# Optimization experiments

Measured on AMD Instinct MI355X. Metric: run time of the kernel, lower is better.

Reference implementation:

```python
import jax, jax.numpy as jnp
import numpy as np

N, E, B = 20000, 160000, 64
NFEAT, NHID, HEADS, NCLASS = 128, 64, 16, 10
GAT_SLOPE = 0.2    # LeakyReLU inside GATv2 attention
OUT_SLOPE = 0.01   # torch.nn.functional.leaky_relu default
TEMPERATURE = 1.0


def _lrelu(x, slope):
    return jnp.where(x >= 0, x, slope * x)


def gatv2_conv(x, src, dst, Wl, bl, Wr, br, att, bias):
    # x: [N, Fin]; PyG GATv2Conv with share_weights=False, concat=False (mean over heads)
    xl = (x @ Wl + bl).reshape(N, HEADS, NHID)   # source-side transform
    xr = (x @ Wr + br).reshape(N, HEADS, NHID)   # target-side transform
    e = _lrelu(xl[src] + xr[dst], GAT_SLOPE)     # [E', H, C] per-edge pre-activation
    logit = jnp.einsum('ehc,hc->eh', e, att)     # [E', H]
    # segment softmax over incoming edges of each target node (self-loops guarantee >=1 edge)
    m = jax.ops.segment_max(logit, dst, num_segments=N)
    m = jnp.where(jnp.isfinite(m), m, 0.0)
    ex = jnp.exp(logit - m[dst])
    den = jax.ops.segment_sum(ex, dst, num_segments=N)
    alpha = ex / den[dst]                        # [E', H]
    out = jax.ops.segment_sum(alpha[:, :, None] * xl[src], dst, num_segments=N)  # [N, H, C]
    return out.mean(axis=1) + bias               # concat=False -> head average, then bias


def setup_inputs() -> dict:
    key = jax.random.key(0)
    ks = jax.random.split(key, 20)
    s = 0.05
    inp = {
        'x': jax.random.normal(ks[0], (N, NFEAT), dtype=jnp.float32),
        'edge_index': jax.random.randint(ks[1], (2, E), 0, N, dtype=jnp.int64)
            if jax.config.jax_enable_x64 else jax.random.randint(ks[1], (2, E), 0, N).astype(jnp.int32),
        'batch': jnp.sort(jax.random.randint(ks[2], (N,), 0, B)).astype(jnp.int32),
        # GATv2 layer 1
        'W1l': jax.random.normal(ks[3], (NFEAT, HEADS * NHID), dtype=jnp.float32) * s,
        'b1l': jnp.zeros((HEADS * NHID,), jnp.float32),
        'W1r': jax.random.normal(ks[4], (NFEAT, HEADS * NHID), dtype=jnp.float32) * s,
        'b1r': jnp.zeros((HEADS * NHID,), jnp.float32),
        'att1': jax.random.normal(ks[5], (HEADS, NHID), dtype=jnp.float32) * s,
        'bias1': jnp.zeros((NHID,), jnp.float32),
        # GATv2 layer 2
        'W2l': jax.random.normal(ks[6], (NHID, HEADS * NHID), dtype=jnp.float32) * s,
        'b2l': jnp.zeros((HEADS * NHID,), jnp.float32),
        'W2r': jax.random.normal(ks[7], (NHID, HEADS * NHID), dtype=jnp.float32) * s,
        'b2r': jnp.zeros((HEADS * NHID,), jnp.float32),
        'att2': jax.random.normal(ks[8], (HEADS, NHID), dtype=jnp.float32) * s,
        'bias2': jnp.zeros((NHID,), jnp.float32),
        # heads
        'Wc': jax.random.normal(ks[9], (NHID, NCLASS), dtype=jnp.float32) * s,
        'bc': jnp.zeros((NCLASS,), jnp.float32),
        'Wv': jax.random.normal(ks[10], (NHID, 1), dtype=jnp.float32) * s,
        'bv': jnp.zeros((1,), jnp.float32),
    }
    return inp


def reference(x, edge_index, batch, W1l, b1l, W1r, b1r, att1, bias1,
              W2l, b2l, W2r, b2r, att2, bias2, Wc, bc, Wv, bv):
    loop = jnp.arange(N, dtype=edge_index.dtype)  # PyG add_self_loops=True
    src = jnp.concatenate([edge_index[0], loop])
    dst = jnp.concatenate([edge_index[1], loop])

    h = _lrelu(gatv2_conv(x, src, dst, W1l, b1l, W1r, b1r, att1, bias1), OUT_SLOPE)
    h = _lrelu(gatv2_conv(h, src, dst, W2l, b2l, W2r, b2r, att2, bias2), OUT_SLOPE)
    # dropout p=0.0 -> identity

    sums = jax.ops.segment_sum(h, batch, num_segments=B)           # [B, NHID]
    cnt = jax.ops.segment_sum(jnp.ones((N,), h.dtype), batch, num_segments=B)
    pooled = sums / jnp.maximum(cnt, 1.0)[:, None]                 # global_mean_pool

    logits = (pooled @ Wc + bc) / TEMPERATURE                      # [B, NCLASS]
    log_var = pooled @ Wv + bv                                     # [B, 1]
    return (logits, log_var)
```

## Files before the change

kernel.cpp:

```cpp
#include <hip/hip_runtime.h>
#include <hip/hip_bf16.h>
#include <hip/hip_fp16.h>
#include <math.h>

#define NN   20000
#define EE   160000
#define NBAT 64
#define NF   128
#define NH   64
#define NHEAD 16
#define NCLS 10
#define ETOT (EE + NN)

typedef __attribute__((ext_vector_type(8))) short short8;
typedef __attribute__((ext_vector_type(8))) _Float16 half8;
typedef __attribute__((ext_vector_type(2))) _Float16 h2;
typedef __attribute__((ext_vector_type(4))) float f32x4;
typedef unsigned short ushort_t;

#if __has_builtin(__builtin_amdgcn_fdot2)
typedef __fp16 fdot2_t __attribute__((ext_vector_type(2)));
static __device__ __forceinline__ float dot2(h2 a, h2 b, float c) {
    return __builtin_amdgcn_fdot2(__builtin_bit_cast(fdot2_t, a),
                                  __builtin_bit_cast(fdot2_t, b), c, false);
}
#else
static __device__ __forceinline__ float dot2(h2 a, h2 b, float c) {
    return c + (float)a.x * (float)b.x + (float)a.y * (float)b.y;
}
#endif

static __device__ __forceinline__ ushort_t f2bf_rn(float x) {
    unsigned u = __builtin_bit_cast(unsigned, x);
    unsigned r = (u + 0x7fffu + ((u >> 16) & 1u)) >> 16;
    return (ushort_t)r;
}
static __device__ __forceinline__ float bf2f(ushort_t u) {
    unsigned v = (unsigned)u << 16;
    return __builtin_bit_cast(float, v);
}

__global__ void k_hist(const int* __restrict__ ei, int* __restrict__ deg) {
    int e = blockIdx.x * 256 + threadIdx.x;
    if (e < EE) atomicAdd(&deg[ei[EE + e]], 1);
}

__global__ void k_scan(const int* __restrict__ deg, int* __restrict__ rowptr,
                       int* __restrict__ cursor, int* __restrict__ csr) {
    const int T = 1024, PER = (NN + T - 1) / T;
    __shared__ int part[T];
    int t = threadIdx.x;
    int local[PER];
    int s = 0;
    #pragma unroll
    for (int i = 0; i < PER; ++i) {
        int idx = t * PER + i;
        int v = (idx < NN) ? deg[idx] : 0;
        local[i] = v; s += v;
    }
    part[t] = s;
    __syncthreads();
    for (int off = 1; off < T; off <<= 1) {
        int v = (t >= off) ? part[t - off] : 0;
        __syncthreads();
        part[t] += v;
        __syncthreads();
    }
    int ex = (t == 0) ? 0 : part[t - 1];
    #pragma unroll
    for (int i = 0; i < PER; ++i) {
        int idx = t * PER + i;
        if (idx < NN) {
            int base = ex + idx;
            rowptr[idx] = base;
            csr[base]   = idx;
            cursor[idx] = base + 1;
            ex += local[i];
        }
    }
    if (t == T - 1) rowptr[NN] = ex + NN;
}

__global__ void k_scatter(const int* __restrict__ ei, int* __restrict__ cursor,
                          int* __restrict__ csr) {
    int e = blockIdx.x * 256 + threadIdx.x;
    if (e >= EE) return;
    int s = ei[e], d = ei[EE + e];
    int pos = atomicAdd(&cursor[d], 1);
    csr[pos] = s;
}

__global__ void k_bounds(const int* __restrict__ batch, int* __restrict__ bstart) {
    int n = blockIdx.x * 256 + threadIdx.x;
    if (n >= NN) return;
    int b = batch[n];
    if (n == 0) for (int bb = 0; bb <= b; ++bb) bstart[bb] = 0;
    int bn = (n + 1 < NN) ? batch[n + 1] : NBAT;
    for (int bb = b + 1; bb <= bn; ++bb) bstart[bb] = n + 1;
}

__global__ void k_split_a(const float* __restrict__ A, ushort_t* __restrict__ hi,
                          ushort_t* __restrict__ lo, int count4) {
    int idx = blockIdx.x * 256 + threadIdx.x;
    if (idx >= count4) return;
    float4 x = *(const float4*)(A + idx * 4);
    ushort4 h, l;
    h.x = f2bf_rn(x.x); l.x = f2bf_rn(x.x - bf2f(h.x));
    h.y = f2bf_rn(x.y); l.y = f2bf_rn(x.y - bf2f(h.y));
    h.z = f2bf_rn(x.z); l.z = f2bf_rn(x.z - bf2f(h.z));
    h.w = f2bf_rn(x.w); l.w = f2bf_rn(x.w - bf2f(h.w));
    *(ushort4*)(hi + idx * 4) = h;
    *(ushort4*)(lo + idx * 4) = l;
}

template<int K>
__global__ void k_split_w(const float* __restrict__ W, ushort_t* __restrict__ hi,
                          ushort_t* __restrict__ lo) {
    int idx = blockIdx.x * 256 + threadIdx.x;
    if (idx >= K * 1024) return;
    int k = idx >> 10, n = idx & 1023;
    float x = W[idx];
    ushort_t h = f2bf_rn(x);
    hi[n * K + k] = h;
    lo[n * K + k] = f2bf_rn(x - bf2f(h));
}

template<int K>
__global__ __launch_bounds__(256) void k_gemm_mfma(
    const ushort_t* __restrict__ Ahi, const ushort_t* __restrict__ Alo, int M,
    const ushort_t* __restrict__ W0hi, const ushort_t* __restrict__ W0lo,
    const float* __restrict__ b0, _Float16* __restrict__ O0,
    const ushort_t* __restrict__ W1hi, const ushort_t* __restrict__ W1lo,
    const float* __restrict__ b1, _Float16* __restrict__ O1)
{
    const ushort_t* Whi = blockIdx.z ? W1hi : W0hi;
    const ushort_t* Wlo = blockIdx.z ? W1lo : W0lo;
    const float*    bi  = blockIdx.z ? b1 : b0;
    _Float16*       O   = blockIdx.z ? O1 : O0;

    const int c0 = blockIdx.x * 128;
    const int r0 = blockIdx.y * 128;

    __shared__ __align__(16) ushort_t As_hi[128 * 64];
    __shared__ __align__(16) ushort_t As_lo[128 * 64];
    __shared__ __align__(16) ushort_t Ws_hi[128 * 64];
    __shared__ __align__(16) ushort_t Ws_lo[128 * 64];

    const int t = threadIdx.x;
    const int lane = t & 63;
    const int wv = t >> 6, wr = wv >> 1, wc = wv & 1;
    const int fr = lane & 15;
    const int k0 = (lane >> 4) * 8;

    f32x4 acc[4][4] = {};

    for (int kt = 0; kt < K; kt += 64) {
        #pragma unroll
        for (int p = 0; p < 4; ++p) {
            int idx = p * 256 + t;
            int m  = idx >> 3;
            int kc = (idx & 7) * 8;
            int gr = r0 + m;
            uint4 vh = make_uint4(0, 0, 0, 0), vl = make_uint4(0, 0, 0, 0);
            if (gr < M) {
                vh = *(const uint4*)(Ahi + (size_t)gr * K + kt + kc);
                vl = *(const uint4*)(Alo + (size_t)gr * K + kt + kc);
            }
            int sw = (m * 128 + kc * 2) ^ ((m & 7) << 4);
            *(uint4*)((char*)As_hi + sw) = vh;
            *(uint4*)((char*)As_lo + sw) = vl;
            uint4 wh = *(const uint4*)(Whi + (size_t)(c0 + m) * K + kt + kc);
            uint4 wl = *(const uint4*)(Wlo + (size_t)(c0 + m) * K + kt + kc);
            *(uint4*)((char*)Ws_hi + sw) = wh;
            *(uint4*)((char*)Ws_lo + sw) = wl;
        }
        __syncthreads();

        #pragma unroll
        for (int ks = 0; ks < 64; ks += 32) {
            short8 ah[4], al[4], bh[4], bl[4];
            #pragma unroll
            for (int i = 0; i < 4; ++i) {
                int row = wr * 64 + i * 16 + fr;
                int off = (row * 128 + (ks + k0) * 2) ^ ((row & 7) << 4);
                ah[i] = *(const short8*)((const char*)As_hi + off);
                al[i] = *(const short8*)((const char*)As_lo + off);
            }
            #pragma unroll
            for (int j = 0; j < 4; ++j) {
                int col = wc * 64 + j * 16 + fr;
                int off = (col * 128 + (ks + k0) * 2) ^ ((col & 7) << 4);
                bh[j] = *(const short8*)((const char*)Ws_hi + off);
                bl[j] = *(const short8*)((const char*)Ws_lo + off);
            }
            #pragma unroll
            for (int i = 0; i < 4; ++i)
                #pragma unroll
                for (int j = 0; j < 4; ++j) {
                    acc[i][j] = __builtin_amdgcn_mfma_f32_16x16x32_bf16(ah[i], bh[j], acc[i][j], 0, 0, 0);
                    acc[i][j] = __builtin_amdgcn_mfma_f32_16x16x32_bf16(ah[i], bl[j], acc[i][j], 0, 0, 0);
                    acc[i][j] = __builtin_amdgcn_mfma_f32_16x16x32_bf16(al[i], bh[j], acc[i][j], 0, 0, 0);
                }
        }
        __syncthreads();
    }

    float bj[4];
    #pragma unroll
    for (int j = 0; j < 4; ++j) bj[j] = bi[c0 + wc * 64 + j * 16 + fr];
    #pragma unroll
    for (int i = 0; i < 4; ++i) {
        int rbase = r0 + wr * 64 + i * 16 + (lane >> 4) * 4;
        #pragma unroll
        for (int r = 0; r < 4; ++r) {
            int gr = rbase + r;
            if (gr < M) {
                #pragma unroll
                for (int j = 0; j < 4; ++j)
                    O[(size_t)gr * 1024 + c0 + wc * 64 + j * 16 + fr] =
                        (_Float16)(acc[i][j][r] + bj[j]);
            }
        }
    }
}

static __device__ __forceinline__ void edge_update(
    half8 a0, half8 a1, half8 xr0, half8 xr1, const h2* att2,
    float& m, float& den, float* acc)
{
    half8 t0 = a0 + xr0;
    half8 t1 = a1 + xr1;
    t0 = __builtin_elementwise_max(t0, t0 * (_Float16)0.2f);
    t1 = __builtin_elementwise_max(t1, t1 * (_Float16)0.2f);
    const h2* p0 = (const h2*)&t0;
    const h2* p1 = (const h2*)&t1;
    float lg = 0.f;
    #pragma unroll
    for (int j = 0; j < 4; ++j) lg = dot2(p0[j], att2[j], lg);
    #pragma unroll
    for (int j = 0; j < 4; ++j) lg = dot2(p1[j], att2[4 + j], lg);
    lg += __shfl_xor(lg, 1);
    lg += __shfl_xor(lg, 2);
    const float nm = fmaxf(m, lg);
    const float p  = __expf(lg - nm);
    const float sc = __expf(m - nm);
    den = den * sc + p;
    const _Float16* xa = (const _Float16*)&a0;
    const _Float16* xb = (const _Float16*)&a1;
    #pragma unroll
    for (int j = 0; j < 8; ++j) acc[j]     = fmaf((float)xa[j], p, acc[j] * sc);
    #pragma unroll
    for (int j = 0; j < 8; ++j) acc[8 + j] = fmaf((float)xb[j], p, acc[8 + j] * sc);
    m = nm;
}

template<int SPLIT>
__global__ __launch_bounds__(256) void k_attn(
    const _Float16* __restrict__ xl, const _Float16* __restrict__ xr,
    const float* __restrict__ att, const float* __restrict__ bias,
    const int* __restrict__ rowptr, const int* __restrict__ csr,
    float* __restrict__ hout, ushort_t* __restrict__ hhi, ushort_t* __restrict__ hlo)
{
    const int wave = threadIdx.x >> 6;
    const int lane = threadIdx.x & 63;
    const int n = blockIdx.x * 4 + wave;
    if (n >= NN) return;
    const int h  = lane >> 2;
    const int cc = lane & 3;
    const int cb = h * NH + cc * 16;

    h2 att2[8];
    #pragma unroll
    for (int i = 0; i < 4; ++i) {
        float4 a = *(const float4*)(att + cb + i * 4);
        att2[i * 2 + 0] = h2{(_Float16)a.x, (_Float16)a.y};
        att2[i * 2 + 1] = h2{(_Float16)a.z, (_Float16)a.w};
    }
    const half8 xr0 = *(const half8*)(xr + (size_t)n * 1024 + cb);
    const half8 xr1 = *(const half8*)(xr + (size_t)n * 1024 + cb + 8);

    float acc[16];
    #pragma unroll
    for (int j = 0; j < 16; ++j) acc[j] = 0.f;
    float m = -INFINITY, den = 0.f;

    const int e0 = rowptr[n], e1 = rowptr[n + 1];
    int e = e0;
    for (; e + 4 <= e1; e += 4) {
        const int s0 = csr[e], s1 = csr[e + 1], s2 = csr[e + 2], s3 = csr[e + 3];
        const _Float16* p0 = xl + (size_t)s0 * 1024 + cb;
        const _Float16* p1 = xl + (size_t)s1 * 1024 + cb;
        const _Float16* p2 = xl + (size_t)s2 * 1024 + cb;
        const _Float16* p3 = xl + (size_t)s3 * 1024 + cb;
        half8 a0 = *(const half8*)p0, a1 = *(const half8*)(p0 + 8);
        half8 b0 = *(const half8*)p1, b1 = *(const half8*)(p1 + 8);
        half8 c0 = *(const half8*)p2, c1 = *(const half8*)(p2 + 8);
        half8 d0 = *(const half8*)p3, d1 = *(const half8*)(p3 + 8);
        edge_update(a0, a1, xr0, xr1, att2, m, den, acc);
        edge_update(b0, b1, xr0, xr1, att2, m, den, acc);
        edge_update(c0, c1, xr0, xr1, att2, m, den, acc);
        edge_update(d0, d1, xr0, xr1, att2, m, den, acc);
    }
    for (; e < e1; ++e) {
        const int s = csr[e];
        const _Float16* p0 = xl + (size_t)s * 1024 + cb;
        half8 a0 = *(const half8*)p0, a1 = *(const half8*)(p0 + 8);
        edge_update(a0, a1, xr0, xr1, att2, m, den, acc);
    }

    const float inv = 1.f / den;
    float v[16];
    #pragma unroll
    for (int j = 0; j < 16; ++j) v[j] = acc[j] * inv;
    #pragma unroll
    for (int mask = 4; mask <= 32; mask <<= 1)
        #pragma unroll
        for (int j = 0; j < 16; ++j) v[j] += __shfl_xor(v[j], mask);

    if (h == 0) {
        float bvv[16];
        #pragma unroll
        for (int i = 0; i < 4; ++i)
            *(float4*)(bvv + i * 4) = *(const float4*)(bias + cc * 16 + i * 4);
        #pragma unroll
        for (int i = 0; i < 4; ++i) {
            float o[4];
            #pragma unroll
            for (int r = 0; r < 4; ++r) {
                float tt = v[i * 4 + r] * 0.0625f + bvv[i * 4 + r];
                o[r] = fmaxf(tt, 0.01f * tt);
            }
            if (SPLIT) {
                ushort4 hh, ll;
                hh.x = f2bf_rn(o[0]); ll.x = f2bf_rn(o[0] - bf2f(hh.x));
                hh.y = f2bf_rn(o[1]); ll.y = f2bf_rn(o[1] - bf2f(hh.y));
                hh.z = f2bf_rn(o[2]); ll.z = f2bf_rn(o[2] - bf2f(hh.z));
                hh.w = f2bf_rn(o[3]); ll.w = f2bf_rn(o[3] - bf2f(hh.w));
                *(ushort4*)(hhi + (size_t)n * NH + cc * 16 + i * 4) = hh;
                *(ushort4*)(hlo + (size_t)n * NH + cc * 16 + i * 4) = ll;
            } else {
                *(float4*)(hout + (size_t)n * NH + cc * 16 + i * 4) =
                    make_float4(o[0], o[1], o[2], o[3]);
            }
        }
    }
}

#define PNODES 128
__global__ __launch_bounds__(256) void k_pool_partial(
    const float* __restrict__ h2buf, const int* __restrict__ batch,
    float* __restrict__ sums)
{
    const int n0 = blockIdx.x * PNODES;
    const int c = threadIdx.x & 63;
    const int r = threadIdx.x >> 6;
    const int nend = (n0 + PNODES < NN) ? n0 + PNODES : NN;
    float s = 0.f;
    int bcur = -1;
    for (int n = n0 + r; n < nend; n += 4) {
        int b = batch[n];
        if (b != bcur) {
            if (bcur >= 0) atomicAdd(&sums[bcur * NH + c], s);
            bcur = b; s = 0.f;
        }
        s += h2buf[(size_t)n * NH + c];
    }
    if (bcur >= 0) atomicAdd(&sums[bcur * NH + c], s);
}

__global__ void k_heads(const float* __restrict__ sums, const int* __restrict__ bstart,
                        const float* __restrict__ Wc, const float* __restrict__ bc,
                        const float* __restrict__ Wv, const float* __restrict__ bv,
                        float* __restrict__ out)
{
    const int b = blockIdx.x, c = threadIdx.x;
    const float cnt = (float)(bstart[b + 1] - bstart[b]);
    const float pooled = sums[b * NH + c] / fmaxf(cnt, 1.f);
    __shared__ float pl[NH];
    pl[c] = pooled;
    __syncthreads();
    if (c < NCLS) {
        float a = bc[c];
        for (int k = 0; k < NH; ++k) a = fmaf(pl[k], Wc[k * NCLS + c], a);
        out[b * NCLS + c] = a;
    } else if (c == NCLS) {
        float a = bv[0];
        for (int k = 0; k < NH; ++k) a = fmaf(pl[k], Wv[k], a);
        out[NBAT * NCLS + b] = a;
    }
}

extern "C" void kernel_launch(void* const* d_in, const int* in_sizes, int n_in,
                              void* d_out, int out_size, void* d_ws, size_t ws_size,
                              hipStream_t stream)
{
    const float* x     = (const float*)d_in[0];
    const int*   ei    = (const int*)  d_in[1];
    const int*   batch = (const int*)  d_in[2];
    const float* W1l = (const float*)d_in[3],  *b1l = (const float*)d_in[4];
    const float* W1r = (const float*)d_in[5],  *b1r = (const float*)d_in[6];
    const float* att1 = (const float*)d_in[7], *bias1 = (const float*)d_in[8];
    const float* W2l = (const float*)d_in[9],  *b2l = (const float*)d_in[10];
    const float* W2r = (const float*)d_in[11], *b2r = (const float*)d_in[12];
    const float* att2 = (const float*)d_in[13], *bias2 = (const float*)d_in[14];
    const float* Wc = (const float*)d_in[15],  *bc = (const float*)d_in[16];
    const float* Wv = (const float*)d_in[17],  *bv = (const float*)d_in[18];
    float* out = (float*)d_out;

    char* ws = (char*)d_ws;
    size_t off = 0;
    auto carve = [&](size_t bytes) {
        char* p = ws + off;
        off = (off + bytes + 255) & ~(size_t)255;
        return p;
    };
    _Float16* xl    = (_Float16*)carve((size_t)NN * 1024 * 2);
    _Float16* xr    = (_Float16*)carve((size_t)NN * 1024 * 2);
    float*    h2b   = (float*)carve((size_t)NN * NH * 4);
    float*    psums = (float*)carve((size_t)NBAT * NH * 4);
    ushort_t* Axhi  = (ushort_t*)carve((size_t)NN * NF * 2);
    ushort_t* Axlo  = (ushort_t*)carve((size_t)NN * NF * 2);
    ushort_t* h1hi  = (ushort_t*)carve((size_t)NN * NH * 2);
    ushort_t* h1lo  = (ushort_t*)carve((size_t)NN * NH * 2);
    ushort_t* Wt1lh = (ushort_t*)carve((size_t)1024 * NF * 2);
    ushort_t* Wt1ll = (ushort_t*)carve((size_t)1024 * NF * 2);
    ushort_t* Wt1rh = (ushort_t*)carve((size_t)1024 * NF * 2);
    ushort_t* Wt1rl = (ushort_t*)carve((size_t)1024 * NF * 2);
    ushort_t* Wt2lh = (ushort_t*)carve((size_t)1024 * NH * 2);
    ushort_t* Wt2ll = (ushort_t*)carve((size_t)1024 * NH * 2);
    ushort_t* Wt2rh = (ushort_t*)carve((size_t)1024 * NH * 2);
    ushort_t* Wt2rl = (ushort_t*)carve((size_t)1024 * NH * 2);
    int*      deg    = (int*)carve((size_t)NN * 4);
    int*      cursor = (int*)carve((size_t)NN * 4);
    int*      rowptr = (int*)carve((size_t)(NN + 1) * 4);
    int*      csr    = (int*)carve((size_t)ETOT * 4);
    int*      bstart = (int*)carve((size_t)(NBAT + 1) * 4);

    hipMemsetAsync(deg, 0, (size_t)NN * 4, stream);
    k_hist   <<<(EE + 255) / 256, 256, 0, stream>>>(ei, deg);
    k_scan   <<<1, 1024, 0, stream>>>(deg, rowptr, cursor, csr);
    k_scatter<<<(EE + 255) / 256, 256, 0, stream>>>(ei, cursor, csr);
    k_bounds <<<(NN + 255) / 256, 256, 0, stream>>>(batch, bstart);

    k_split_a<<<(NN * NF / 4 + 255) / 256, 256, 0, stream>>>(x, Axhi, Axlo, NN * NF / 4);
    k_split_w<NF><<<(NF * 1024 + 255) / 256, 256, 0, stream>>>(W1l, Wt1lh, Wt1ll);
    k_split_w<NF><<<(NF * 1024 + 255) / 256, 256, 0, stream>>>(W1r, Wt1rh, Wt1rl);
    k_split_w<NH><<<(NH * 1024 + 255) / 256, 256, 0, stream>>>(W2l, Wt2lh, Wt2ll);
    k_split_w<NH><<<(NH * 1024 + 255) / 256, 256, 0, stream>>>(W2r, Wt2rh, Wt2rl);

    const int MB = (NN + 127) / 128;
    k_gemm_mfma<NF><<<dim3(8, MB, 2), 256, 0, stream>>>(
        Axhi, Axlo, NN, Wt1lh, Wt1ll, b1l, xl, Wt1rh, Wt1rl, b1r, xr);
    k_attn<1><<<NN / 4, 256, 0, stream>>>(xl, xr, att1, bias1, rowptr, csr,
                                          (float*)nullptr, h1hi, h1lo);
    k_gemm_mfma<NH><<<dim3(8, MB, 2), 256, 0, stream>>>(
        h1hi, h1lo, NN, Wt2lh, Wt2ll, b2l, xl, Wt2rh, Wt2rl, b2r, xr);
    k_attn<0><<<NN / 4, 256, 0, stream>>>(xl, xr, att2, bias2, rowptr, csr,
                                          h2b, (ushort_t*)nullptr, (ushort_t*)nullptr);
    hipMemsetAsync(psums, 0, (size_t)NBAT * NH * 4, stream);
    k_pool_partial<<<(NN + PNODES - 1) / PNODES, 256, 0, stream>>>(h2b, batch, psums);
    k_heads<<<NBAT, NH, 0, stream>>>(psums, bstart, Wc, bc, Wv, bv, out);
}
```

Baseline: 394.4 us.

## Fuse input bf16 split into GEMM, batch weight splits, drop online softmax max

Layer-1 GEMM now reads fp32 x directly and splits it into bf16 hi/lo in the tile loader, removing the separate split kernel and its intermediate buffers. The four weight-split launches are merged into one launch. GEMM grid order is swapped so blocks iterate rows fastest. The attention kernel drops the running-max online softmax, gathers 8 edges per iteration with clamped indices, and accumulates exp(logit) directly. That removes rescaling work but risks overflow if logits grow large, since it relies on small logits.

```diff
diff --git a/kernel.cpp b/kernel.cpp
--- a/kernel.cpp
+++ b/kernel.cpp
@@ -14,18 +14,18 @@
 
 typedef __attribute__((ext_vector_type(8))) short short8;
 typedef __attribute__((ext_vector_type(8))) _Float16 half8;
-typedef __attribute__((ext_vector_type(2))) _Float16 h2;
+typedef __attribute__((ext_vector_type(2))) _Float16 h2v;
 typedef __attribute__((ext_vector_type(4))) float f32x4;
 typedef unsigned short ushort_t;
 
 #if __has_builtin(__builtin_amdgcn_fdot2)
 typedef __fp16 fdot2_t __attribute__((ext_vector_type(2)));
-static __device__ __forceinline__ float dot2(h2 a, h2 b, float c) {
+static __device__ __forceinline__ float dot2(h2v a, h2v b, float c) {
     return __builtin_amdgcn_fdot2(__builtin_bit_cast(fdot2_t, a),
                                   __builtin_bit_cast(fdot2_t, b), c, false);
 }
 #else
-static __device__ __forceinline__ float dot2(h2 a, h2 b, float c) {
+static __device__ __forceinline__ float dot2(h2v a, h2v b, float c) {
     return c + (float)a.x * (float)b.x + (float)a.y * (float)b.y;
 }
 #endif
@@ -99,23 +99,18 @@
     for (int bb = b + 1; bb <= bn; ++bb) bstart[bb] = n + 1;
 }
 
-__global__ void k_split_a(const float* __restrict__ A, ushort_t* __restrict__ hi,
-                          ushort_t* __restrict__ lo, int count4) {
-    int idx = blockIdx.x * 256 + threadIdx.x;
-    if (idx >= count4) return;
-    float4 x = *(const float4*)(A + idx * 4);
-    ushort4 h, l;
-    h.x = f2bf_rn(x.x); l.x = f2bf_rn(x.x - bf2f(h.x));
-    h.y = f2bf_rn(x.y); l.y = f2bf_rn(x.y - bf2f(h.y));
-    h.z = f2bf_rn(x.z); l.z = f2bf_rn(x.z - bf2f(h.z));
-    h.w = f2bf_rn(x.w); l.w = f2bf_rn(x.w - bf2f(h.w));
-    *(ushort4*)(hi + idx * 4) = h;
-    *(ushort4*)(lo + idx * 4) = l;
-}
-
-template<int K>
-__global__ void k_split_w(const float* __restrict__ W, ushort_t* __restrict__ hi,
-                          ushort_t* __restrict__ lo) {
+__global__ void k_split_w4(
+    const float* __restrict__ W0, ushort_t* __restrict__ h0, ushort_t* __restrict__ l0,
+    const float* __restrict__ W1, ushort_t* __restrict__ h1, ushort_t* __restrict__ l1,
+    const float* __restrict__ W2, ushort_t* __restrict__ h2p, ushort_t* __restrict__ l2,
+    const float* __restrict__ W3, ushort_t* __restrict__ h3, ushort_t* __restrict__ l3)
+{
+    const int z = blockIdx.y;
+    const float* W; ushort_t* hi; ushort_t* lo; int K;
+    if      (z == 0) { W = W0; hi = h0;  lo = l0; K = NF; }
+    else if (z == 1) { W = W1; hi = h1;  lo = l1; K = NF; }
+    else if (z == 2) { W = W2; hi = h2p; lo = l2; K = NH; }
+    else             { W = W3; hi = h3;  lo = l3; K = NH; }
     int idx = blockIdx.x * 256 + threadIdx.x;
     if (idx >= K * 1024) return;
     int k = idx >> 10, n = idx & 1023;
@@ -125,6 +120,117 @@
     lo[n * K + k] = f2bf_rn(x - bf2f(h));
 }
 
+
+template<int K>
+__global__ __launch_bounds__(256) void k_gemm_l1(
+    const float* __restrict__ X, int M,
+    const ushort_t* __restrict__ W0hi, const ushort_t* __restrict__ W0lo,
+    const float* __restrict__ b0, _Float16* __restrict__ O0,
+    const ushort_t* __restrict__ W1hi, const ushort_t* __restrict__ W1lo,
+    const float* __restrict__ b1, _Float16* __restrict__ O1)
+{
+    const ushort_t* Whi = blockIdx.z ? W1hi : W0hi;
+    const ushort_t* Wlo = blockIdx.z ? W1lo : W0lo;
+    const float*    bi  = blockIdx.z ? b1 : b0;
+    _Float16*       O   = blockIdx.z ? O1 : O0;
+
+    const int r0 = blockIdx.x * 128;
+    const int c0 = blockIdx.y * 128;
+
+    __shared__ __align__(16) ushort_t As_hi[128 * 64];
+    __shared__ __align__(16) ushort_t As_lo[128 * 64];
+    __shared__ __align__(16) ushort_t Ws_hi[128 * 64];
+    __shared__ __align__(16) ushort_t Ws_lo[128 * 64];
+
+    const int t = threadIdx.x;
+    const int lane = t & 63;
+    const int wv = t >> 6, wr = wv >> 1, wc = wv & 1;
+    const int fr = lane & 15;
+    const int k0 = (lane >> 4) * 8;
+
+    f32x4 acc[4][4] = {};
+
+    for (int kt = 0; kt < K; kt += 64) {
+        #pragma unroll
+        for (int p = 0; p < 4; ++p) {
+            int idx = p * 256 + t;
+            int m  = idx >> 3;
+            int kc = (idx & 7) * 8;
+            int gr = r0 + m;
+            uint4 H = make_uint4(0, 0, 0, 0), L = make_uint4(0, 0, 0, 0);
+            if (gr < M) {
+                float4 v0 = *(const float4*)(X + (size_t)gr * K + kt + kc);
+                float4 v1 = *(const float4*)(X + (size_t)gr * K + kt + kc + 4);
+                float vv[8] = {v0.x, v0.y, v0.z, v0.w, v1.x, v1.y, v1.z, v1.w};
+                unsigned hh[8], ll[8];
+                #pragma unroll
+                for (int q = 0; q < 8; ++q) {
+                    hh[q] = f2bf_rn(vv[q]);
+                    ll[q] = f2bf_rn(vv[q] - bf2f((ushort_t)hh[q]));
+                }
+                H = make_uint4(hh[0] | (hh[1] << 16), hh[2] | (hh[3] << 16),
+                               hh[4] | (hh[5] << 16), hh[6] | (hh[7] << 16));
+                L = make_uint4(ll[0] | (ll[1] << 16), ll[2] | (ll[3] << 16),
+                               ll[4] | (ll[5] << 16), ll[6] | (ll[7] << 16));
+            }
+            int sw = (m * 128 + kc * 2) ^ ((m & 7) << 4);
+            *(uint4*)((char*)As_hi + sw) = H;
+            *(uint4*)((char*)As_lo + sw) = L;
+            uint4 wh = *(const uint4*)(Whi + (size_t)(c0 + m) * K + kt + kc);
+            uint4 wl = *(const uint4*)(Wlo + (size_t)(c0 + m) * K + kt + kc);
+            *(uint4*)((char*)Ws_hi + sw) = wh;
+            *(uint4*)((char*)Ws_lo + sw) = wl;
+        }
+        __syncthreads();
+
+        #pragma unroll
+        for (int ks = 0; ks < 64; ks += 32) {
+            short8 ah[4], al[4], bh[4], bl[4];
+            #pragma unroll
+            for (int i = 0; i < 4; ++i) {
+                int row = wr * 64 + i * 16 + fr;
+                int off = (row * 128 + (ks + k0) * 2) ^ ((row & 7) << 4);
+                ah[i] = *(const short8*)((const char*)As_hi + off);
+                al[i] = *(const short8*)((const char*)As_lo + off);
+            }
+            #pragma unroll
+            for (int j = 0; j < 4; ++j) {
+                int col = wc * 64 + j * 16 + fr;
+                int off = (col * 128 + (ks + k0) * 2) ^ ((col & 7) << 4);
+                bh[j] = *(const short8*)((const char*)Ws_hi + off);
+                bl[j] = *(const short8*)((const char*)Ws_lo + off);
+            }
+            #pragma unroll
+            for (int i = 0; i < 4; ++i)
+                #pragma unroll
+                for (int j = 0; j < 4; ++j) {
+                    acc[i][j] = __builtin_amdgcn_mfma_f32_16x16x32_bf16(ah[i], bh[j], acc[i][j], 0, 0, 0);
+                    acc[i][j] = __builtin_amdgcn_mfma_f32_16x16x32_bf16(ah[i], bl[j], acc[i][j], 0, 0, 0);
+                    acc[i][j] = __builtin_amdgcn_mfma_f32_16x16x32_bf16(al[i], bh[j], acc[i][j], 0, 0, 0);
+                }
+        }
+        __syncthreads();
+    }
+
+    float bj[4];
+    #pragma unroll
+    for (int j = 0; j < 4; ++j) bj[j] = bi[c0 + wc * 64 + j * 16 + fr];
+    #pragma unroll
+    for (int i = 0; i < 4; ++i) {
+        int rbase = r0 + wr * 64 + i * 16 + (lane >> 4) * 4;
+        #pragma unroll
+        for (int r = 0; r < 4; ++r) {
+            int gr = rbase + r;
+            if (gr < M) {
+                #pragma unroll
+                for (int j = 0; j < 4; ++j)
+                    O[(size_t)gr * 1024 + c0 + wc * 64 + j * 16 + fr] =
+                        (_Float16)(acc[i][j][r] + bj[j]);
+            }
+        }
+    }
+}
+
 template<int K>
 __global__ __launch_bounds__(256) void k_gemm_mfma(
     const ushort_t* __restrict__ Ahi, const ushort_t* __restrict__ Alo, int M,
@@ -138,8 +244,8 @@
     const float*    bi  = blockIdx.z ? b1 : b0;
     _Float16*       O   = blockIdx.z ? O1 : O0;
 
-    const int c0 = blockIdx.x * 128;
-    const int r0 = blockIdx.y * 128;
+    const int r0 = blockIdx.x * 128;
+    const int c0 = blockIdx.y * 128;
 
     __shared__ __align__(16) ushort_t As_hi[128 * 64];
     __shared__ __align__(16) ushort_t As_lo[128 * 64];
@@ -224,34 +330,21 @@
     }
 }
 
-static __device__ __forceinline__ void edge_update(
-    half8 a0, half8 a1, half8 xr0, half8 xr1, const h2* att2,
-    float& m, float& den, float* acc)
+static __device__ __forceinline__ float logit8(
+    half8 a0, half8 a1, half8 xr0, half8 xr1, const h2v* att2)
 {
     half8 t0 = a0 + xr0;
     half8 t1 = a1 + xr1;
     t0 = __builtin_elementwise_max(t0, t0 * (_Float16)0.2f);
     t1 = __builtin_elementwise_max(t1, t1 * (_Float16)0.2f);
-    const h2* p0 = (const h2*)&t0;
-    const h2* p1 = (const h2*)&t1;
+    const h2v* p0 = (const h2v*)&t0;
+    const h2v* p1 = (const h2v*)&t1;
     float lg = 0.f;
     #pragma unroll
     for (int j = 0; j < 4; ++j) lg = dot2(p0[j], att2[j], lg);
     #pragma unroll
     for (int j = 0; j < 4; ++j) lg = dot2(p1[j], att2[4 + j], lg);
-    lg += __shfl_xor(lg, 1);
-    lg += __shfl_xor(lg, 2);
-    const float nm = fmaxf(m, lg);
-    const float p  = __expf(lg - nm);
-    const float sc = __expf(m - nm);
-    den = den * sc + p;
-    const _Float16* xa = (const _Float16*)&a0;
-    const _Float16* xb = (const _Float16*)&a1;
-    #pragma unroll
-    for (int j = 0; j < 8; ++j) acc[j]     = fmaf((float)xa[j], p, acc[j] * sc);
-    #pragma unroll
-    for (int j = 0; j < 8; ++j) acc[8 + j] = fmaf((float)xb[j], p, acc[8 + j] * sc);
-    m = nm;
+    return lg;
 }
 
 template<int SPLIT>
@@ -269,12 +362,12 @@
     const int cc = lane & 3;
     const int cb = h * NH + cc * 16;
 
-    h2 att2[8];
+    h2v att2[8];
     #pragma unroll
     for (int i = 0; i < 4; ++i) {
         float4 a = *(const float4*)(att + cb + i * 4);
-        att2[i * 2 + 0] = h2{(_Float16)a.x, (_Float16)a.y};
-        att2[i * 2 + 1] = h2{(_Float16)a.z, (_Float16)a.w};
+        att2[i * 2 + 0] = h2v{(_Float16)a.x, (_Float16)a.y};
+        att2[i * 2 + 1] = h2v{(_Float16)a.z, (_Float16)a.w};
     }
     const half8 xr0 = *(const half8*)(xr + (size_t)n * 1024 + cb);
     const half8 xr1 = *(const half8*)(xr + (size_t)n * 1024 + cb + 8);
@@ -282,30 +375,37 @@
     float acc[16];
     #pragma unroll
     for (int j = 0; j < 16; ++j) acc[j] = 0.f;
-    float m = -INFINITY, den = 0.f;
+    float den = 0.f;
 
     const int e0 = rowptr[n], e1 = rowptr[n + 1];
-    int e = e0;
-    for (; e + 4 <= e1; e += 4) {
-        const int s0 = csr[e], s1 = csr[e + 1], s2 = csr[e + 2], s3 = csr[e + 3];
-        const _Float16* p0 = xl + (size_t)s0 * 1024 + cb;
-        const _Float16* p1 = xl + (size_t)s1 * 1024 + cb;
-        const _Float16* p2 = xl + (size_t)s2 * 1024 + cb;
-        const _Float16* p3 = xl + (size_t)s3 * 1024 + cb;
-        half8 a0 = *(const half8*)p0, a1 = *(const half8*)(p0 + 8);
-        half8 b0 = *(const half8*)p1, b1 = *(const half8*)(p1 + 8);
-        half8 c0 = *(const half8*)p2, c1 = *(const half8*)(p2 + 8);
-        half8 d0 = *(const half8*)p3, d1 = *(const half8*)(p3 + 8);
-        edge_update(a0, a1, xr0, xr1, att2, m, den, acc);
-        edge_update(b0, b1, xr0, xr1, att2, m, den, acc);
-        edge_update(c0, c1, xr0, xr1, att2, m, den, acc);
-        edge_update(d0, d1, xr0, xr1, att2, m, den, acc);
-    }
-    for (; e < e1; ++e) {
-        const int s = csr[e];
-        const _Float16* p0 = xl + (size_t)s * 1024 + cb;
-        half8 a0 = *(const half8*)p0, a1 = *(const half8*)(p0 + 8);
-        edge_update(a0, a1, xr0, xr1, att2, m, den, acc);
+    for (int e = e0; e < e1; e += 8) {
+        int src[8];
+        #pragma unroll
+        for (int j = 0; j < 8; ++j) {
+            int ee = e + j;
+            src[j] = csr[(ee < e1) ? ee : (e1 - 1)];
+        }
+        half8 xa0[8], xa1[8];
+        #pragma unroll
+        for (int j = 0; j < 8; ++j) {
+            const _Float16* p = xl + (size_t)src[j] * 1024 + cb;
+            xa0[j] = *(const half8*)p;
+            xa1[j] = *(const half8*)(p + 8);
+        }
+        #pragma unroll
+        for (int j = 0; j < 8; ++j) {
+            float lg = logit8(xa0[j], xa1[j], xr0, xr1, att2);
+            lg += __shfl_xor(lg, 1);
+            lg += __shfl_xor(lg, 2);
+            float p = (e + j < e1) ? __expf(lg) : 0.f;
+            den += p;
+            const _Float16* va = (const _Float16*)&xa0[j];
+            const _Float16* vb = (const _Float16*)&xa1[j];
+            #pragma unroll
+            for (int q = 0; q < 8; ++q) acc[q]     = fmaf((float)va[q], p, acc[q]);
+            #pragma unroll
+            for (int q = 0; q < 8; ++q) acc[8 + q] = fmaf((float)vb[q], p, acc[8 + q]);
+        }
     }
 
     const float inv = 1.f / den;
@@ -418,8 +518,6 @@
     _Float16* xr    = (_Float16*)carve((size_t)NN * 1024 * 2);
     float*    h2b   = (float*)carve((size_t)NN * NH * 4);
     float*    psums = (float*)carve((size_t)NBAT * NH * 4);
-    ushort_t* Axhi  = (ushort_t*)carve((size_t)NN * NF * 2);
-    ushort_t* Axlo  = (ushort_t*)carve((size_t)NN * NF * 2);
     ushort_t* h1hi  = (ushort_t*)carve((size_t)NN * NH * 2);
     ushort_t* h1lo  = (ushort_t*)carve((size_t)NN * NH * 2);
     ushort_t* Wt1lh = (ushort_t*)carve((size_t)1024 * NF * 2);
@@ -442,18 +540,16 @@
     k_scatter<<<(EE + 255) / 256, 256, 0, stream>>>(ei, cursor, csr);
     k_bounds <<<(NN + 255) / 256, 256, 0, stream>>>(batch, bstart);
 
-    k_split_a<<<(NN * NF / 4 + 255) / 256, 256, 0, stream>>>(x, Axhi, Axlo, NN * NF / 4);
-    k_split_w<NF><<<(NF * 1024 + 255) / 256, 256, 0, stream>>>(W1l, Wt1lh, Wt1ll);
-    k_split_w<NF><<<(NF * 1024 + 255) / 256, 256, 0, stream>>>(W1r, Wt1rh, Wt1rl);
-    k_split_w<NH><<<(NH * 1024 + 255) / 256, 256, 0, stream>>>(W2l, Wt2lh, Wt2ll);
-    k_split_w<NH><<<(NH * 1024 + 255) / 256, 256, 0, stream>>>(W2r, Wt2rh, Wt2rl);
+    k_split_w4<<<dim3((NF * 1024 + 255) / 256, 4), 256, 0, stream>>>(
+        W1l, Wt1lh, Wt1ll, W1r, Wt1rh, Wt1rl,
+        W2l, Wt2lh, Wt2ll, W2r, Wt2rh, Wt2rl);
 
     const int MB = (NN + 127) / 128;
-    k_gemm_mfma<NF><<<dim3(8, MB, 2), 256, 0, stream>>>(
-        Axhi, Axlo, NN, Wt1lh, Wt1ll, b1l, xl, Wt1rh, Wt1rl, b1r, xr);
+    k_gemm_l1<NF><<<dim3(MB, 8, 2), 256, 0, stream>>>(
+        x, NN, Wt1lh, Wt1ll, b1l, xl, Wt1rh, Wt1rl, b1r, xr);
     k_attn<1><<<NN / 4, 256, 0, stream>>>(xl, xr, att1, bias1, rowptr, csr,
                                           (float*)nullptr, h1hi, h1lo);
-    k_gemm_mfma<NH><<<dim3(8, MB, 2), 256, 0, stream>>>(
+    k_gemm_mfma<NH><<<dim3(MB, 8, 2), 256, 0, stream>>>(
         h1hi, h1lo, NN, Wt2lh, Wt2ll, b2l, xl, Wt2rh, Wt2rl, b2r, xr);
     k_attn<0><<<NN / 4, 256, 0, stream>>>(xl, xr, att2, bias2, rowptr, csr,
                                           h2b, (ushort_t*)nullptr, (ushort_t*)nullptr);
```

Result: slower. 453.3 us (+14.9%).
